# Kernel optimization log

Hardware: AMD Instinct MI355X
Metric: run time of the kernel (lower is better)

## Reference

```python
import jax, jax.numpy as jnp
import numpy as np

N_NODES = 100000
N_EDGES = 1250000
HID = 64
IN_CH = 64
OUT_CH = 16
N_GRAPHS = 512


def setup_inputs() -> dict:
    key = jax.random.key(0)
    ks = jax.random.split(key, 20)
    x = jax.random.normal(ks[0], (N_NODES, IN_CH), dtype=jnp.float32)
    edge_index = jax.random.randint(ks[1], (2, N_EDGES), 0, N_NODES, dtype=jnp.int64)
    batch = jnp.sort(jax.random.randint(ks[2], (N_NODES,), 0, N_GRAPHS, dtype=jnp.int64))
    s_in = 1.0 / np.sqrt(IN_CH)
    s_h = 1.0 / np.sqrt(HID)
    u = lambda k, shp, s: jax.random.uniform(k, shp, jnp.float32, -s, s)
    return {
        "x": x, "edge_index": edge_index, "batch": batch,
        "W0": u(ks[3], (IN_CH, HID), s_in), "b0": u(ks[4], (HID,), s_in),
        "W1a": u(ks[5], (HID, HID), s_h), "b1a": u(ks[6], (HID,), s_h),
        "W1b": u(ks[7], (HID, HID), s_h), "b1b": u(ks[8], (HID,), s_h),
        "W2a": u(ks[9], (HID, HID), s_h), "b2a": u(ks[10], (HID,), s_h),
        "W2b": u(ks[11], (HID, HID), s_h), "b2b": u(ks[12], (HID,), s_h),
        "W3a": u(ks[13], (HID, HID), s_h), "b3a": u(ks[14], (HID,), s_h),
        "W3b": u(ks[15], (HID, HID), s_h), "b3b": u(ks[16], (HID,), s_h),
        "Wl": u(ks[17], (HID, OUT_CH), s_h), "bl": u(ks[18], (OUT_CH,), s_h),
    }


def _gin_conv(h, src, dst, Wa, ba, Wb, bb):
    # GINConv, eps=0: mlp(x_i + sum_{j->i} x_j); mlp = Linear,ReLU,Linear
    agg = jax.ops.segment_sum(h[src], dst, num_segments=N_NODES)  # [N, HID]
    z = h + agg
    return jax.nn.relu(z @ Wa + ba) @ Wb + bb


def reference(x, edge_index, batch, W0, b0, W1a, b1a, W1b, b1b,
              W2a, b2a, W2b, b2b, W3a, b3a, W3b, b3b, Wl, bl):
    src, dst = edge_index[0], edge_index[1]
    h = jax.nn.relu(x @ W0 + b0)
    h = jax.nn.relu(_gin_conv(h, src, dst, W1a, b1a, W1b, b1b))
    h = jax.nn.relu(_gin_conv(h, src, dst, W2a, b2a, W2b, b2b))
    h = jax.nn.relu(_gin_conv(h, src, dst, W3a, b3a, W3b, b3b))
    # global mean pool over graphs
    sums = jax.ops.segment_sum(h, batch, num_segments=N_GRAPHS)  # [G, HID]
    cnts = jax.ops.segment_sum(jnp.ones((N_NODES,), h.dtype), batch, num_segments=N_GRAPHS)
    pooled = sums / jnp.maximum(cnts, 1.0)[:, None]
    # dropout p=0.5 is identity in eval mode
    return pooled @ Wl + bl  # [G, OUT_CH]
```

## Files before the change

### kernel.cpp

```cpp
#include <hip/hip_runtime.h>
#include <hip/hip_fp16.h>

#define N_NODES 100000
#define N_EDGES 1250000
#define HID 64
#define N_GRAPHS 512
#define OUT_CH 16

#define NSUP 196
#define SB_CAP 8192
#define E_BLK 2048
#define NPB ((N_EDGES + E_BLK - 1) / E_BLK)
#define TILE2 ((N_NODES + 127) / 128)
#define TSTRIDE 68

typedef _Float16 h16;
typedef _Float16 half2_t __attribute__((ext_vector_type(2)));
typedef _Float16 f16x8 __attribute__((ext_vector_type(8)));
typedef float f32x4 __attribute__((ext_vector_type(4)));

__device__ __forceinline__ void acc4(uint2 u, float& a0, float& a1, float& a2, float& a3) {
    half2_t h0 = __builtin_bit_cast(half2_t, u.x);
    half2_t h1 = __builtin_bit_cast(half2_t, u.y);
    a0 += (float)h0[0];
    a1 += (float)h0[1];
    a2 += (float)h1[0];
    a3 += (float)h1[1];
}

__device__ __forceinline__ unsigned pack2(float x, float y) {
    half2_t o;
    o[0] = (h16)x;
    o[1] = (h16)y;
    return __builtin_bit_cast(unsigned, o);
}

__global__ __launch_bounds__(256) void k_partition(const int* __restrict__ src,
                                                   const int* __restrict__ dst,
                                                   int* __restrict__ cnt,
                                                   int* __restrict__ buckets) {
    __shared__ int hist[256];
    __shared__ int gbase[256];
    __shared__ int tsum[256];
    __shared__ int stage[E_BLK];
    int t = threadIdx.x;
    int e0 = blockIdx.x * E_BLK;
    int eN = N_EDGES - e0;
    if (eN > E_BLK) eN = E_BLK;

    hist[t] = 0;
    __syncthreads();
    for (int i = t; i < eN; i += 256) atomicAdd(&hist[dst[e0 + i] >> 9], 1);
    __syncthreads();

    int c = hist[t];
    tsum[t] = c;
    __syncthreads();
    for (int off = 1; off < 256; off <<= 1) {
        int u = (t >= off) ? tsum[t - off] : 0;
        __syncthreads();
        tsum[t] += u;
        __syncthreads();
    }
    int pref = tsum[t] - c;
    if (t < NSUP && c > 0) gbase[t] = atomicAdd(&cnt[t], c);
    hist[t] = pref;
    __syncthreads();

    for (int i = t; i < eN; i += 256) {
        int s = src[e0 + i];
        int d = dst[e0 + i];
        int p = atomicAdd(&hist[d >> 9], 1);
        stage[p] = ((d & 511) << 17) | s;
    }
    __syncthreads();

    if (t < NSUP && c > 0) {
        int lstart = hist[t] - c;
        int gb = gbase[t];
        int cap = SB_CAP - gb;
        int n = c < cap ? c : (cap > 0 ? cap : 0);
        int* dp = buckets + (size_t)t * SB_CAP + gb;
        int r = 0;
        while (r < n && (((size_t)(dp + r)) & 15)) { dp[r] = stage[lstart + r]; ++r; }
        for (; r + 4 <= n; r += 4) {
            int4 v;
            v.x = stage[lstart + r];
            v.y = stage[lstart + r + 1];
            v.z = stage[lstart + r + 2];
            v.w = stage[lstart + r + 3];
            *(int4*)(dp + r) = v;
        }
        for (; r < n; ++r) dp[r] = stage[lstart + r];
    }
}

__global__ __launch_bounds__(256) void k_sort(const int* __restrict__ cnt,
                                              int* __restrict__ buckets,
                                              int* __restrict__ rowptrS) {
    __shared__ int srt[SB_CAP];
    __shared__ int hist[512];
    __shared__ int curs[512];
    __shared__ int tsum[256];
    int s = blockIdx.x, t = threadIdx.x;
    int n = cnt[s];
    n = n < SB_CAP ? n : SB_CAP;
    int* gb = buckets + (size_t)s * SB_CAP;
    int sBase = s * SB_CAP;

    hist[t] = 0;
    hist[t + 256] = 0;
    __syncthreads();
    for (int i = t; i < n; i += 256) atomicAdd(&hist[gb[i] >> 17], 1);
    __syncthreads();

    int c0 = hist[2 * t], c1 = hist[2 * t + 1];
    int tot = c0 + c1;
    tsum[t] = tot;
    __syncthreads();
    for (int off = 1; off < 256; off <<= 1) {
        int u = (t >= off) ? tsum[t - off] : 0;
        __syncthreads();
        tsum[t] += u;
        __syncthreads();
    }
    int pref = tsum[t] - tot;
    curs[2 * t] = pref;
    curs[2 * t + 1] = pref + c0;
    rowptrS[s * 513 + 2 * t] = sBase + pref;
    rowptrS[s * 513 + 2 * t + 1] = sBase + pref + c0;
    if (t == 255) rowptrS[s * 513 + 512] = sBase + n;
    __syncthreads();

    for (int i = t; i < n; i += 256) {
        int rec = gb[i];
        int pos = atomicAdd(&curs[rec >> 17], 1);
        srt[pos] = rec;
    }
    __syncthreads();
    for (int i = t; i < n; i += 256) gb[i] = srt[i];
}

__global__ __launch_bounds__(256) void k_aggregate(const int* __restrict__ rowptrS,
                                                   const int* __restrict__ buckets,
                                                   const h16* __restrict__ H,
                                                   h16* __restrict__ Z) {
    const uint2* H4 = (const uint2*)H;
    uint2* Z4 = (uint2*)Z;
    int lane = threadIdx.x & 63;
    int part = lane >> 4, sub = lane & 15;
    int gwave = (blockIdx.x * 256 + threadIdx.x) >> 6;
    int nw = (gridDim.x * 256) >> 6;
    for (int i0 = gwave * 4; i0 < N_NODES; i0 += nw * 4) {
        int i = i0 + part;
        bool valid = i < N_NODES;
        int iv = valid ? i : N_NODES - 1;
        int s = iv >> 9, l = iv & 511;
        int start = rowptrS[s * 513 + l];
        int end = valid ? rowptrS[s * 513 + l + 1] : start;
        float a0 = 0.f, a1 = 0.f, a2 = 0.f, a3 = 0.f;
        acc4(H4[(size_t)iv * 16 + sub], a0, a1, a2, a3);
        int j = start;
        for (; j + 8 <= end; j += 8) {
            int s0 = buckets[j] & 0x1FFFF;
            int s1 = buckets[j + 1] & 0x1FFFF;
            int s2 = buckets[j + 2] & 0x1FFFF;
            int s3 = buckets[j + 3] & 0x1FFFF;
            int s4 = buckets[j + 4] & 0x1FFFF;
            int s5 = buckets[j + 5] & 0x1FFFF;
            int s6 = buckets[j + 6] & 0x1FFFF;
            int s7 = buckets[j + 7] & 0x1FFFF;
            uint2 u0 = H4[(size_t)s0 * 16 + sub];
            uint2 u1 = H4[(size_t)s1 * 16 + sub];
            uint2 u2 = H4[(size_t)s2 * 16 + sub];
            uint2 u3 = H4[(size_t)s3 * 16 + sub];
            uint2 u4 = H4[(size_t)s4 * 16 + sub];
            uint2 u5 = H4[(size_t)s5 * 16 + sub];
            uint2 u6 = H4[(size_t)s6 * 16 + sub];
            uint2 u7 = H4[(size_t)s7 * 16 + sub];
            acc4(u0, a0, a1, a2, a3);
            acc4(u1, a0, a1, a2, a3);
            acc4(u2, a0, a1, a2, a3);
            acc4(u3, a0, a1, a2, a3);
            acc4(u4, a0, a1, a2, a3);
            acc4(u5, a0, a1, a2, a3);
            acc4(u6, a0, a1, a2, a3);
            acc4(u7, a0, a1, a2, a3);
        }
        if (j + 4 <= end) {
            int s0 = buckets[j] & 0x1FFFF;
            int s1 = buckets[j + 1] & 0x1FFFF;
            int s2 = buckets[j + 2] & 0x1FFFF;
            int s3 = buckets[j + 3] & 0x1FFFF;
            uint2 u0 = H4[(size_t)s0 * 16 + sub];
            uint2 u1 = H4[(size_t)s1 * 16 + sub];
            uint2 u2 = H4[(size_t)s2 * 16 + sub];
            uint2 u3 = H4[(size_t)s3 * 16 + sub];
            acc4(u0, a0, a1, a2, a3);
            acc4(u1, a0, a1, a2, a3);
            acc4(u2, a0, a1, a2, a3);
            acc4(u3, a0, a1, a2, a3);
            j += 4;
        }
        if (j + 2 <= end) {
            int s0 = buckets[j] & 0x1FFFF;
            int s1 = buckets[j + 1] & 0x1FFFF;
            uint2 u0 = H4[(size_t)s0 * 16 + sub];
            uint2 u1 = H4[(size_t)s1 * 16 + sub];
            acc4(u0, a0, a1, a2, a3);
            acc4(u1, a0, a1, a2, a3);
            j += 2;
        }
        if (j < end) {
            int s0 = buckets[j] & 0x1FFFF;
            acc4(H4[(size_t)s0 * 16 + sub], a0, a1, a2, a3);
        }
        if (valid) {
            uint2 o;
            o.x = pack2(a0, a1);
            o.y = pack2(a2, a3);
            Z4[(size_t)i * 16 + sub] = o;
        }
    }
}

__global__ __launch_bounds__(256) void k_wprep(const float* __restrict__ Wq0,
                                               const float* __restrict__ Wq1,
                                               const float* __restrict__ Wq2,
                                               const float* __restrict__ Wq3,
                                               const float* __restrict__ Wq4,
                                               const float* __restrict__ Wq5,
                                               const float* __restrict__ Wq6,
                                               h16* __restrict__ WF) {
    const float* Ws[7] = {Wq0, Wq1, Wq2, Wq3, Wq4, Wq5, Wq6};
    const float* W = Ws[blockIdx.x];
    h16* dstW = WF + (size_t)blockIdx.x * 4096;
    int t = threadIdx.x;
#pragma unroll
    for (int i = 0; i < 16; ++i) {
        int s = t + 256 * i;
        int k = s >> 6, col = s & 63;
        int kc = k >> 5, quad = (k >> 3) & 3, j = k & 7;
        int c = col >> 4, n = col & 15;
        dstW[((c * 2 + kc) * 4 + quad) * 128 + n * 8 + j] = (h16)W[s];
    }
}

__global__ __launch_bounds__(256) void k_mlp(const h16* __restrict__ WaF,
                                             const float* __restrict__ Ba,
                                             const h16* __restrict__ WbF,
                                             const float* __restrict__ Bb,
                                             const h16* __restrict__ Zin,
                                             h16* __restrict__ Hout) {
    __shared__ float sT[4 * 16 * TSTRIDE];
    int t = threadIdx.x;
    int w = t >> 6, lane = t & 63;
    int n16 = lane & 15, quad = lane >> 4;
    float* T = sT + w * 16 * TSTRIDE;

    f16x8 bwa[4][2], bwb[4][2];
#pragma unroll
    for (int c = 0; c < 4; ++c)
#pragma unroll
        for (int kc = 0; kc < 2; ++kc) {
            int f = ((c * 2 + kc) * 4 + quad) * 128 + n16 * 8;
            bwa[c][kc] = *(const f16x8*)(WaF + f);
            bwb[c][kc] = *(const f16x8*)(WbF + f);
        }
    float bva[4], bvb[4];
#pragma unroll
    for (int c = 0; c < 4; ++c) {
        bva[c] = Ba[c * 16 + n16];
        bvb[c] = Bb[c * 16 + n16];
    }

#pragma unroll
    for (int tt = 0; tt < 2; ++tt) {
        int rbase = blockIdx.x * 128 + tt * 64 + w * 16;
        int arow = rbase + n16;
        int crow = arow < N_NODES ? arow : N_NODES - 1;
        const f16x8* zp = (const f16x8*)(Zin + (size_t)crow * HID + quad * 8);
        f16x8 a0 = zp[0];
        f16x8 a1 = zp[4];

        f32x4 acc[4];
#pragma unroll
        for (int c = 0; c < 4; ++c) {
            acc[c] = (f32x4){bva[c], bva[c], bva[c], bva[c]};
            acc[c] = __builtin_amdgcn_mfma_f32_16x16x32_f16(a0, bwa[c][0], acc[c], 0, 0, 0);
            acc[c] = __builtin_amdgcn_mfma_f32_16x16x32_f16(a1, bwa[c][1], acc[c], 0, 0, 0);
        }

#pragma unroll
        for (int c = 0; c < 4; ++c)
#pragma unroll
            for (int r = 0; r < 4; ++r)
                T[(quad * 4 + r) * TSTRIDE + c * 16 + n16] = fmaxf(acc[c][r], 0.f);

        f16x8 ta[2];
#pragma unroll
        for (int kc = 0; kc < 2; ++kc) {
            float4 p = *(const float4*)&T[n16 * TSTRIDE + kc * 32 + quad * 8];
            float4 q = *(const float4*)&T[n16 * TSTRIDE + kc * 32 + quad * 8 + 4];
            f16x8 v;
            v[0] = (h16)p.x; v[1] = (h16)p.y; v[2] = (h16)p.z; v[3] = (h16)p.w;
            v[4] = (h16)q.x; v[5] = (h16)q.y; v[6] = (h16)q.z; v[7] = (h16)q.w;
            ta[kc] = v;
        }

#pragma unroll
        for (int c = 0; c < 4; ++c) {
            acc[c] = (f32x4){bvb[c], bvb[c], bvb[c], bvb[c]};
            acc[c] = __builtin_amdgcn_mfma_f32_16x16x32_f16(ta[0], bwb[c][0], acc[c], 0, 0, 0);
            acc[c] = __builtin_amdgcn_mfma_f32_16x16x32_f16(ta[1], bwb[c][1], acc[c], 0, 0, 0);
        }

#pragma unroll
        for (int c = 0; c < 4; ++c)
#pragma unroll
            for (int r = 0; r < 4; ++r)
                T[(quad * 4 + r) * TSTRIDE + c * 16 + n16] = fmaxf(acc[c][r], 0.f);
        {
            int rl = lane >> 2, seg = lane & 3;
            int row = rbase + rl;
            if (row < N_NODES) {
                const float* tr = &T[rl * TSTRIDE + seg * 16];
                f16x8 o0, o1;
#pragma unroll
                for (int i = 0; i < 8; ++i) {
                    o0[i] = (h16)tr[i];
                    o1[i] = (h16)tr[8 + i];
                }
                f16x8* dp = (f16x8*)(Hout + (size_t)row * HID + seg * 16);
                dp[0] = o0;
                dp[1] = o1;
            }
        }
    }
}

__global__ __launch_bounds__(256) void k_lin(const h16* __restrict__ W0F,
                                             const float* __restrict__ B,
                                             const float* __restrict__ Xin,
                                             h16* __restrict__ Hout) {
    __shared__ float sT[4 * 16 * TSTRIDE];
    int t = threadIdx.x;
    int w = t >> 6, lane = t & 63;
    int n16 = lane & 15, quad = lane >> 4;
    float* T = sT + w * 16 * TSTRIDE;

    f16x8 bw[4][2];
#pragma unroll
    for (int c = 0; c < 4; ++c)
#pragma unroll
        for (int kc = 0; kc < 2; ++kc)
            bw[c][kc] = *(const f16x8*)(W0F + ((c * 2 + kc) * 4 + quad) * 128 + n16 * 8);
    float bv[4];
#pragma unroll
    for (int c = 0; c < 4; ++c) bv[c] = B[c * 16 + n16];

#pragma unroll
    for (int tt = 0; tt < 2; ++tt) {
        int rbase = blockIdx.x * 128 + tt * 64 + w * 16;
        int arow = rbase + n16;
        int crow = arow < N_NODES ? arow : N_NODES - 1;
        f16x8 a[2];
#pragma unroll
        for (int kc = 0; kc < 2; ++kc) {
            const float4* xp = (const float4*)(Xin + (size_t)crow * HID + kc * 32 + quad * 8);
            float4 p = xp[0], q = xp[1];
            f16x8 v;
            v[0] = (h16)p.x; v[1] = (h16)p.y; v[2] = (h16)p.z; v[3] = (h16)p.w;
            v[4] = (h16)q.x; v[5] = (h16)q.y; v[6] = (h16)q.z; v[7] = (h16)q.w;
            a[kc] = v;
        }

        f32x4 acc[4];
#pragma unroll
        for (int c = 0; c < 4; ++c) {
            acc[c] = (f32x4){bv[c], bv[c], bv[c], bv[c]};
#pragma unroll
            for (int kc = 0; kc < 2; ++kc)
                acc[c] = __builtin_amdgcn_mfma_f32_16x16x32_f16(a[kc], bw[c][kc], acc[c], 0, 0, 0);
        }

#pragma unroll
        for (int c = 0; c < 4; ++c)
#pragma unroll
            for (int r = 0; r < 4; ++r)
                T[(quad * 4 + r) * TSTRIDE + c * 16 + n16] = fmaxf(acc[c][r], 0.f);
        {
            int rl = lane >> 2, seg = lane & 3;
            int row = rbase + rl;
            if (row < N_NODES) {
                const float* tr = &T[rl * TSTRIDE + seg * 16];
                f16x8 o0, o1;
#pragma unroll
                for (int i = 0; i < 8; ++i) {
                    o0[i] = (h16)tr[i];
                    o1[i] = (h16)tr[8 + i];
                }
                f16x8* dp = (f16x8*)(Hout + (size_t)row * HID + seg * 16);
                dp[0] = o0;
                dp[1] = o1;
            }
        }
    }
}

__global__ __launch_bounds__(256) void k_poolfinal(const h16* __restrict__ H,
                                                   const int* __restrict__ batch,
                                                   const float* __restrict__ Wl,
                                                   const float* __restrict__ bl,
                                                   float* __restrict__ out) {
    __shared__ float sp[4 * HID];
    int g = blockIdx.x;
    int t = threadIdx.x;
    int lane = t & 63, w = t >> 6;
    int lo = 0, hi = N_NODES;
    while (lo < hi) { int m = (lo + hi) >> 1; if (batch[m] < g) lo = m + 1; else hi = m; }
    int start = lo;
    hi = N_NODES;
    while (lo < hi) { int m = (lo + hi) >> 1; if (batch[m] < g + 1) lo = m + 1; else hi = m; }
    int end = lo;
    float s0 = 0.f, s1 = 0.f, s2 = 0.f, s3 = 0.f;
    int r = start + w;
    for (; r + 12 < end; r += 16) {
        float v0 = (float)H[(size_t)r * HID + lane];
        float v1 = (float)H[(size_t)(r + 4) * HID + lane];
        float v2 = (float)H[(size_t)(r + 8) * HID + lane];
        float v3 = (float)H[(size_t)(r + 12) * HID + lane];
        s0 += v0; s1 += v1; s2 += v2; s3 += v3;
    }
    for (; r < end; r += 4) s0 += (float)H[(size_t)r * HID + lane];
    sp[w * HID + lane] = s0 + s1 + s2 + s3;
    __syncthreads();
    if (t < HID) {
        float tot = sp[t] + sp[HID + t] + sp[2 * HID + t] + sp[3 * HID + t];
        float c = (end > start) ? (float)(end - start) : 1.0f;
        sp[t] = tot / c;
    }
    __syncthreads();
    if (t < OUT_CH) {
        float acc = bl[t];
#pragma unroll
        for (int k = 0; k < HID; ++k) acc += sp[k] * Wl[k * OUT_CH + t];
        out[g * OUT_CH + t] = acc;
    }
}

extern "C" void kernel_launch(void* const* d_in, const int* in_sizes, int n_in,
                              void* d_out, int out_size, void* d_ws, size_t ws_size,
                              hipStream_t stream) {
    const float* x     = (const float*)d_in[0];
    const int*   edge  = (const int*)d_in[1];
    const int*   batch = (const int*)d_in[2];
    const float* W0  = (const float*)d_in[3];
    const float* b0  = (const float*)d_in[4];
    const float* W1a = (const float*)d_in[5];
    const float* b1a = (const float*)d_in[6];
    const float* W1b = (const float*)d_in[7];
    const float* b1b = (const float*)d_in[8];
    const float* W2a = (const float*)d_in[9];
    const float* b2a = (const float*)d_in[10];
    const float* W2b = (const float*)d_in[11];
    const float* b2b = (const float*)d_in[12];
    const float* W3a = (const float*)d_in[13];
    const float* b3a = (const float*)d_in[14];
    const float* W3b = (const float*)d_in[15];
    const float* b3b = (const float*)d_in[16];
    const float* Wl  = (const float*)d_in[17];
    const float* bl  = (const float*)d_in[18];
    float* out = (float*)d_out;

    const int* src = edge;
    const int* dst = edge + N_EDGES;

    h16* HA = (h16*)d_ws;
    h16* Z  = HA + (size_t)N_NODES * HID;
    int* cnt     = (int*)(Z + (size_t)N_NODES * HID);
    int* rowptrS = cnt + NSUP;
    int* buckets = rowptrS + NSUP * 513;
    h16* WF      = (h16*)(buckets + (size_t)NSUP * SB_CAP);
    h16* W0F = WF;
    h16* W1aF = WF + 4096 * 1;
    h16* W1bF = WF + 4096 * 2;
    h16* W2aF = WF + 4096 * 3;
    h16* W2bF = WF + 4096 * 4;
    h16* W3aF = WF + 4096 * 5;
    h16* W3bF = WF + 4096 * 6;

    hipMemsetAsync(cnt, 0, NSUP * sizeof(int), stream);
    k_partition<<<NPB, 256, 0, stream>>>(src, dst, cnt, buckets);
    k_sort<<<NSUP, 256, 0, stream>>>(cnt, buckets, rowptrS);
    k_wprep<<<7, 256, 0, stream>>>(W0, W1a, W1b, W2a, W2b, W3a, W3b, WF);

    k_lin<<<TILE2, 256, 0, stream>>>(W0F, b0, x, HA);

    k_aggregate<<<6250, 256, 0, stream>>>(rowptrS, buckets, HA, Z);
    k_mlp<<<TILE2, 256, 0, stream>>>(W1aF, b1a, W1bF, b1b, Z, HA);

    k_aggregate<<<6250, 256, 0, stream>>>(rowptrS, buckets, HA, Z);
    k_mlp<<<TILE2, 256, 0, stream>>>(W2aF, b2a, W2bF, b2b, Z, HA);

    k_aggregate<<<6250, 256, 0, stream>>>(rowptrS, buckets, HA, Z);
    k_mlp<<<TILE2, 256, 0, stream>>>(W3aF, b3a, W3bF, b3b, Z, HA);

    k_poolfinal<<<N_GRAPHS, 256, 0, stream>>>(HA, batch, Wl, bl, out);
}
```

Baseline: 285.2 us.

## Fuse aggregation with GIN MLP and merge setup kernels into one launch

```diff
diff --git a/kernel.cpp b/kernel.cpp
--- a/kernel.cpp
+++ b/kernel.cpp
@@ -12,6 +12,7 @@
 #define E_BLK 2048
 #define NPB ((N_EDGES + E_BLK - 1) / E_BLK)
 #define TILE2 ((N_NODES + 127) / 128)
+#define NWP 6
 #define TSTRIDE 68
 
 typedef _Float16 h16;
@@ -35,63 +36,160 @@
     return __builtin_bit_cast(unsigned, o);
 }
 
-__global__ __launch_bounds__(256) void k_partition(const int* __restrict__ src,
-                                                   const int* __restrict__ dst,
-                                                   int* __restrict__ cnt,
-                                                   int* __restrict__ buckets) {
+__global__ __launch_bounds__(256) void k_fat(const int* __restrict__ src,
+                                             const int* __restrict__ dst,
+                                             int* __restrict__ cnt,
+                                             int* __restrict__ buckets,
+                                             const float* __restrict__ W1a,
+                                             const float* __restrict__ W1b,
+                                             const float* __restrict__ W2a,
+                                             const float* __restrict__ W2b,
+                                             const float* __restrict__ W3a,
+                                             const float* __restrict__ W3b,
+                                             h16* __restrict__ WF,
+                                             const float* __restrict__ W0,
+                                             const float* __restrict__ B0,
+                                             const float* __restrict__ Xin,
+                                             h16* __restrict__ Hout) {
     __shared__ int hist[256];
     __shared__ int gbase[256];
     __shared__ int tsum[256];
-    __shared__ int stage[E_BLK];
+    __shared__ __align__(16) int stage[E_BLK];
+    __shared__ __align__(16) float sT[4 * 16 * TSTRIDE];
+
+    int b = blockIdx.x;
     int t = threadIdx.x;
-    int e0 = blockIdx.x * E_BLK;
-    int eN = N_EDGES - e0;
-    if (eN > E_BLK) eN = E_BLK;
-
-    hist[t] = 0;
-    __syncthreads();
-    for (int i = t; i < eN; i += 256) atomicAdd(&hist[dst[e0 + i] >> 9], 1);
-    __syncthreads();
-
-    int c = hist[t];
-    tsum[t] = c;
-    __syncthreads();
-    for (int off = 1; off < 256; off <<= 1) {
-        int u = (t >= off) ? tsum[t - off] : 0;
-        __syncthreads();
-        tsum[t] += u;
-        __syncthreads();
-    }
-    int pref = tsum[t] - c;
-    if (t < NSUP && c > 0) gbase[t] = atomicAdd(&cnt[t], c);
-    hist[t] = pref;
-    __syncthreads();
-
-    for (int i = t; i < eN; i += 256) {
-        int s = src[e0 + i];
-        int d = dst[e0 + i];
-        int p = atomicAdd(&hist[d >> 9], 1);
-        stage[p] = ((d & 511) << 17) | s;
-    }
-    __syncthreads();
-
-    if (t < NSUP && c > 0) {
-        int lstart = hist[t] - c;
-        int gb = gbase[t];
-        int cap = SB_CAP - gb;
-        int n = c < cap ? c : (cap > 0 ? cap : 0);
-        int* dp = buckets + (size_t)t * SB_CAP + gb;
-        int r = 0;
-        while (r < n && (((size_t)(dp + r)) & 15)) { dp[r] = stage[lstart + r]; ++r; }
-        for (; r + 4 <= n; r += 4) {
-            int4 v;
-            v.x = stage[lstart + r];
-            v.y = stage[lstart + r + 1];
-            v.z = stage[lstart + r + 2];
-            v.w = stage[lstart + r + 3];
-            *(int4*)(dp + r) = v;
-        }
-        for (; r < n; ++r) dp[r] = stage[lstart + r];
+
+    if (b < NPB) {
+        int e0 = b * E_BLK;
+        int eN = N_EDGES - e0;
+        if (eN > E_BLK) eN = E_BLK;
+
+        hist[t] = 0;
+        __syncthreads();
+        for (int i = t; i < eN; i += 256) atomicAdd(&hist[dst[e0 + i] >> 9], 1);
+        __syncthreads();
+
+        int c = hist[t];
+        tsum[t] = c;
+        __syncthreads();
+        for (int off = 1; off < 256; off <<= 1) {
+            int u = (t >= off) ? tsum[t - off] : 0;
+            __syncthreads();
+            tsum[t] += u;
+            __syncthreads();
+        }
+        int pref = tsum[t] - c;
+        if (t < NSUP && c > 0) gbase[t] = atomicAdd(&cnt[t], c);
+        hist[t] = pref;
+        __syncthreads();
+
+        for (int i = t; i < eN; i += 256) {
+            int s = src[e0 + i];
+            int d = dst[e0 + i];
+            int p = atomicAdd(&hist[d >> 9], 1);
+            stage[p] = ((d & 511) << 17) | s;
+        }
+        __syncthreads();
+
+        if (t < NSUP && c > 0) {
+            int lstart = hist[t] - c;
+            int gb = gbase[t];
+            int cap = SB_CAP - gb;
+            int n = c < cap ? c : (cap > 0 ? cap : 0);
+            int* dp = buckets + (size_t)t * SB_CAP + gb;
+            int r = 0;
+            while (r < n && (((size_t)(dp + r)) & 15)) { dp[r] = stage[lstart + r]; ++r; }
+            for (; r + 4 <= n; r += 4) {
+                int4 v;
+                v.x = stage[lstart + r];
+                v.y = stage[lstart + r + 1];
+                v.z = stage[lstart + r + 2];
+                v.w = stage[lstart + r + 3];
+                *(int4*)(dp + r) = v;
+            }
+            for (; r < n; ++r) dp[r] = stage[lstart + r];
+        }
+    } else if (b < NPB + NWP) {
+        const float* Ws[NWP] = {W1a, W1b, W2a, W2b, W3a, W3b};
+        const float* W = Ws[b - NPB];
+        h16* dstW = WF + (size_t)(b - NPB) * 4096;
+#pragma unroll
+        for (int i = 0; i < 16; ++i) {
+            int s = t + 256 * i;
+            int k = s >> 6, col = s & 63;
+            int kc = k >> 5, quad = (k >> 3) & 3, j = k & 7;
+            int c = col >> 4, n = col & 15;
+            dstW[((c * 2 + kc) * 4 + quad) * 128 + n * 8 + j] = (h16)W[s];
+        }
+    } else {
+        int lb = b - NPB - NWP;
+        int w = t >> 6, lane = t & 63;
+        int n16 = lane & 15, quad = lane >> 4;
+        float* T = sT + w * 16 * TSTRIDE;
+
+        f16x8 bw[4][2];
+#pragma unroll
+        for (int c = 0; c < 4; ++c)
+#pragma unroll
+            for (int kc = 0; kc < 2; ++kc) {
+                f16x8 v;
+#pragma unroll
+                for (int j = 0; j < 8; ++j)
+                    v[j] = (h16)W0[(kc * 32 + quad * 8 + j) * 64 + c * 16 + n16];
+                bw[c][kc] = v;
+            }
+        float bv[4];
+#pragma unroll
+        for (int c = 0; c < 4; ++c) bv[c] = B0[c * 16 + n16];
+
+#pragma unroll
+        for (int tt = 0; tt < 2; ++tt) {
+            int rbase = lb * 128 + tt * 64 + w * 16;
+            int arow = rbase + n16;
+            int crow = arow < N_NODES ? arow : N_NODES - 1;
+            f16x8 a[2];
+#pragma unroll
+            for (int kc = 0; kc < 2; ++kc) {
+                const float4* xp = (const float4*)(Xin + (size_t)crow * HID + kc * 32 + quad * 8);
+                float4 p = xp[0], q = xp[1];
+                f16x8 v;
+                v[0] = (h16)p.x; v[1] = (h16)p.y; v[2] = (h16)p.z; v[3] = (h16)p.w;
+                v[4] = (h16)q.x; v[5] = (h16)q.y; v[6] = (h16)q.z; v[7] = (h16)q.w;
+                a[kc] = v;
+            }
+
+            f32x4 acc[4];
+#pragma unroll
+            for (int c = 0; c < 4; ++c) {
+                acc[c] = (f32x4){bv[c], bv[c], bv[c], bv[c]};
+#pragma unroll
+                for (int kc = 0; kc < 2; ++kc)
+                    acc[c] = __builtin_amdgcn_mfma_f32_16x16x32_f16(a[kc], bw[c][kc], acc[c], 0, 0, 0);
+            }
+
+#pragma unroll
+            for (int c = 0; c < 4; ++c)
+#pragma unroll
+                for (int r = 0; r < 4; ++r)
+                    T[(quad * 4 + r) * TSTRIDE + c * 16 + n16] = fmaxf(acc[c][r], 0.f);
+            {
+                int rl = lane >> 2, seg = lane & 3;
+                int row = rbase + rl;
+                if (row < N_NODES) {
+                    const float* tr = &T[rl * TSTRIDE + seg * 16];
+                    f16x8 o0, o1;
+#pragma unroll
+                    for (int i = 0; i < 8; ++i) {
+                        o0[i] = (h16)tr[i];
+                        o1[i] = (h16)tr[8 + i];
+                    }
+                    f16x8* dp = (f16x8*)(Hout + (size_t)row * HID + seg * 16);
+                    dp[0] = o0;
+                    dp[1] = o1;
+                }
+            }
+        }
     }
 }
 
@@ -141,20 +239,27 @@
     for (int i = t; i < n; i += 256) gb[i] = srt[i];
 }
 
-__global__ __launch_bounds__(256) void k_aggregate(const int* __restrict__ rowptrS,
-                                                   const int* __restrict__ buckets,
-                                                   const h16* __restrict__ H,
-                                                   h16* __restrict__ Z) {
-    const uint2* H4 = (const uint2*)H;
-    uint2* Z4 = (uint2*)Z;
-    int lane = threadIdx.x & 63;
+__global__ __launch_bounds__(256) void k_aggmlp(const int* __restrict__ rowptrS,
+                                                const int* __restrict__ buckets,
+                                                const h16* __restrict__ WaF,
+                                                const float* __restrict__ Ba,
+                                                const h16* __restrict__ WbF,
+                                                const float* __restrict__ Bb,
+                                                const h16* __restrict__ Hin,
+                                                h16* __restrict__ Hout) {
+    __shared__ __align__(16) float sT[4 * 16 * TSTRIDE];
+    char* zb = (char*)sT;
+    const uint2* H4 = (const uint2*)Hin;
+    int t = threadIdx.x;
+    int w = t >> 6, lane = t & 63;
     int part = lane >> 4, sub = lane & 15;
-    int gwave = (blockIdx.x * 256 + threadIdx.x) >> 6;
-    int nw = (gridDim.x * 256) >> 6;
-    for (int i0 = gwave * 4; i0 < N_NODES; i0 += nw * 4) {
-        int i = i0 + part;
-        bool valid = i < N_NODES;
-        int iv = valid ? i : N_NODES - 1;
+    int n16 = lane & 15, quad = lane >> 4;
+
+    for (int it = 0; it < 8; ++it) {
+        int rloc = it * 16 + w * 4 + part;
+        int grow = blockIdx.x * 128 + rloc;
+        bool valid = grow < N_NODES;
+        int iv = valid ? grow : N_NODES - 1;
         int s = iv >> 9, l = iv & 511;
         int start = rowptrS[s * 513 + l];
         int end = valid ? rowptrS[s * 513 + l + 1] : start;
@@ -215,48 +320,22 @@
             int s0 = buckets[j] & 0x1FFFF;
             acc4(H4[(size_t)s0 * 16 + sub], a0, a1, a2, a3);
         }
-        if (valid) {
-            uint2 o;
-            o.x = pack2(a0, a1);
-            o.y = pack2(a2, a3);
-            Z4[(size_t)i * 16 + sub] = o;
-        }
-    }
-}
-
-__global__ __launch_bounds__(256) void k_wprep(const float* __restrict__ Wq0,
-                                               const float* __restrict__ Wq1,
-                                               const float* __restrict__ Wq2,
-                                               const float* __restrict__ Wq3,
-                                               const float* __restrict__ Wq4,
-                                               const float* __restrict__ Wq5,
-                                               const float* __restrict__ Wq6,
-                                               h16* __restrict__ WF) {
-    const float* Ws[7] = {Wq0, Wq1, Wq2, Wq3, Wq4, Wq5, Wq6};
-    const float* W = Ws[blockIdx.x];
-    h16* dstW = WF + (size_t)blockIdx.x * 4096;
-    int t = threadIdx.x;
-#pragma unroll
-    for (int i = 0; i < 16; ++i) {
-        int s = t + 256 * i;
-        int k = s >> 6, col = s & 63;
-        int kc = k >> 5, quad = (k >> 3) & 3, j = k & 7;
-        int c = col >> 4, n = col & 15;
-        dstW[((c * 2 + kc) * 4 + quad) * 128 + n * 8 + j] = (h16)W[s];
-    }
-}
-
-__global__ __launch_bounds__(256) void k_mlp(const h16* __restrict__ WaF,
-                                             const float* __restrict__ Ba,
-                                             const h16* __restrict__ WbF,
-                                             const float* __restrict__ Bb,
-                                             const h16* __restrict__ Zin,
-                                             h16* __restrict__ Hout) {
-    __shared__ float sT[4 * 16 * TSTRIDE];
-    int t = threadIdx.x;
-    int w = t >> 6, lane = t & 63;
-    int n16 = lane & 15, quad = lane >> 4;
-    float* T = sT + w * 16 * TSTRIDE;
+        uint2 o;
+        o.x = pack2(a0, a1);
+        o.y = pack2(a2, a3);
+        int zoff = (rloc * 128 + sub * 8) ^ ((rloc & 7) << 4);
+        *(uint2*)(zb + zoff) = o;
+    }
+    __syncthreads();
+
+    f16x8 afr[2][2];
+#pragma unroll
+    for (int tt = 0; tt < 2; ++tt) {
+        int rl = tt * 64 + w * 16 + n16;
+        int swz = (rl & 7) << 4;
+        afr[tt][0] = *(const f16x8*)(zb + ((rl * 128 + quad * 16) ^ swz));
+        afr[tt][1] = *(const f16x8*)(zb + ((rl * 128 + 64 + quad * 16) ^ swz));
+    }
 
     f16x8 bwa[4][2], bwb[4][2];
 #pragma unroll
@@ -273,22 +352,19 @@
         bva[c] = Ba[c * 16 + n16];
         bvb[c] = Bb[c * 16 + n16];
     }
-
+    __syncthreads();
+
+    float* T = sT + w * 16 * TSTRIDE;
 #pragma unroll
     for (int tt = 0; tt < 2; ++tt) {
         int rbase = blockIdx.x * 128 + tt * 64 + w * 16;
-        int arow = rbase + n16;
-        int crow = arow < N_NODES ? arow : N_NODES - 1;
-        const f16x8* zp = (const f16x8*)(Zin + (size_t)crow * HID + quad * 8);
-        f16x8 a0 = zp[0];
-        f16x8 a1 = zp[4];
 
         f32x4 acc[4];
 #pragma unroll
         for (int c = 0; c < 4; ++c) {
             acc[c] = (f32x4){bva[c], bva[c], bva[c], bva[c]};
-            acc[c] = __builtin_amdgcn_mfma_f32_16x16x32_f16(a0, bwa[c][0], acc[c], 0, 0, 0);
-            acc[c] = __builtin_amdgcn_mfma_f32_16x16x32_f16(a1, bwa[c][1], acc[c], 0, 0, 0);
+            acc[c] = __builtin_amdgcn_mfma_f32_16x16x32_f16(afr[tt][0], bwa[c][0], acc[c], 0, 0, 0);
+            acc[c] = __builtin_amdgcn_mfma_f32_16x16x32_f16(afr[tt][1], bwa[c][1], acc[c], 0, 0, 0);
         }
 
 #pragma unroll
@@ -313,75 +389,6 @@
             acc[c] = (f32x4){bvb[c], bvb[c], bvb[c], bvb[c]};
             acc[c] = __builtin_amdgcn_mfma_f32_16x16x32_f16(ta[0], bwb[c][0], acc[c], 0, 0, 0);
             acc[c] = __builtin_amdgcn_mfma_f32_16x16x32_f16(ta[1], bwb[c][1], acc[c], 0, 0, 0);
-        }
-
-#pragma unroll
-        for (int c = 0; c < 4; ++c)
-#pragma unroll
-            for (int r = 0; r < 4; ++r)
-                T[(quad * 4 + r) * TSTRIDE + c * 16 + n16] = fmaxf(acc[c][r], 0.f);
-        {
-            int rl = lane >> 2, seg = lane & 3;
-            int row = rbase + rl;
-            if (row < N_NODES) {
-                const float* tr = &T[rl * TSTRIDE + seg * 16];
-                f16x8 o0, o1;
-#pragma unroll
-                for (int i = 0; i < 8; ++i) {
-                    o0[i] = (h16)tr[i];
-                    o1[i] = (h16)tr[8 + i];
-                }
-                f16x8* dp = (f16x8*)(Hout + (size_t)row * HID + seg * 16);
-                dp[0] = o0;
-                dp[1] = o1;
-            }
-        }
-    }
-}
-
-__global__ __launch_bounds__(256) void k_lin(const h16* __restrict__ W0F,
-                                             const float* __restrict__ B,
-                                             const float* __restrict__ Xin,
-                                             h16* __restrict__ Hout) {
-    __shared__ float sT[4 * 16 * TSTRIDE];
-    int t = threadIdx.x;
-    int w = t >> 6, lane = t & 63;
-    int n16 = lane & 15, quad = lane >> 4;
-    float* T = sT + w * 16 * TSTRIDE;
-
-    f16x8 bw[4][2];
-#pragma unroll
-    for (int c = 0; c < 4; ++c)
-#pragma unroll
-        for (int kc = 0; kc < 2; ++kc)
-            bw[c][kc] = *(const f16x8*)(W0F + ((c * 2 + kc) * 4 + quad) * 128 + n16 * 8);
-    float bv[4];
-#pragma unroll
-    for (int c = 0; c < 4; ++c) bv[c] = B[c * 16 + n16];
-
-#pragma unroll
-    for (int tt = 0; tt < 2; ++tt) {
-        int rbase = blockIdx.x * 128 + tt * 64 + w * 16;
-        int arow = rbase + n16;
-        int crow = arow < N_NODES ? arow : N_NODES - 1;
-        f16x8 a[2];
-#pragma unroll
-        for (int kc = 0; kc < 2; ++kc) {
-            const float4* xp = (const float4*)(Xin + (size_t)crow * HID + kc * 32 + quad * 8);
-            float4 p = xp[0], q = xp[1];
-            f16x8 v;
-            v[0] = (h16)p.x; v[1] = (h16)p.y; v[2] = (h16)p.z; v[3] = (h16)p.w;
-            v[4] = (h16)q.x; v[5] = (h16)q.y; v[6] = (h16)q.z; v[7] = (h16)q.w;
-            a[kc] = v;
-        }
-
-        f32x4 acc[4];
-#pragma unroll
-        for (int c = 0; c < 4; ++c) {
-            acc[c] = (f32x4){bv[c], bv[c], bv[c], bv[c]};
-#pragma unroll
-            for (int kc = 0; kc < 2; ++kc)
-                acc[c] = __builtin_amdgcn_mfma_f32_16x16x32_f16(a[kc], bw[c][kc], acc[c], 0, 0, 0);
         }
 
 #pragma unroll
@@ -477,34 +484,26 @@
     const int* dst = edge + N_EDGES;
 
     h16* HA = (h16*)d_ws;
-    h16* Z  = HA + (size_t)N_NODES * HID;
-    int* cnt     = (int*)(Z + (size_t)N_NODES * HID);
+    h16* HB = HA + (size_t)N_NODES * HID;
+    int* cnt     = (int*)(HB + (size_t)N_NODES * HID);
     int* rowptrS = cnt + NSUP;
     int* buckets = rowptrS + NSUP * 513;
     h16* WF      = (h16*)(buckets + (size_t)NSUP * SB_CAP);
-    h16* W0F = WF;
-    h16* W1aF = WF + 4096 * 1;
-    h16* W1bF = WF + 4096 * 2;
-    h16* W2aF = WF + 4096 * 3;
-    h16* W2bF = WF + 4096 * 4;
-    h16* W3aF = WF + 4096 * 5;
-    h16* W3bF = WF + 4096 * 6;
+    h16* W1aF = WF;
+    h16* W1bF = WF + 4096 * 1;
+    h16* W2aF = WF + 4096 * 2;
+    h16* W2bF = WF + 4096 * 3;
+    h16* W3aF = WF + 4096 * 4;
+    h16* W3bF = WF + 4096 * 5;
 
     hipMemsetAsync(cnt, 0, NSUP * sizeof(int), stream);
-    k_partition<<<NPB, 256, 0, stream>>>(src, dst, cnt, buckets);
+    k_fat<<<NPB + NWP + TILE2, 256, 0, stream>>>(src, dst, cnt, buckets,
+        W1a, W1b, W2a, W2b, W3a, W3b, WF, W0, b0, x, HA);
     k_sort<<<NSUP, 256, 0, stream>>>(cnt, buckets, rowptrS);
-    k_wprep<<<7, 256, 0, stream>>>(W0, W1a, W1b, W2a, W2b, W3a, W3b, WF);
-
-    k_lin<<<TILE2, 256, 0, stream>>>(W0F, b0, x, HA);
-
-    k_aggregate<<<6250, 256, 0, stream>>>(rowptrS, buckets, HA, Z);
-    k_mlp<<<TILE2, 256, 0, stream>>>(W1aF, b1a, W1bF, b1b, Z, HA);
-
-    k_aggregate<<<6250, 256, 0, stream>>>(rowptrS, buckets, HA, Z);
-    k_mlp<<<TILE2, 256, 0, stream>>>(W2aF, b2a, W2bF, b2b, Z, HA);
-
-    k_aggregate<<<6250, 256, 0, stream>>>(rowptrS, buckets, HA, Z);
-    k_mlp<<<TILE2, 256, 0, stream>>>(W3aF, b3a, W3bF, b3b, Z, HA);
-
-    k_poolfinal<<<N_GRAPHS, 256, 0, stream>>>(HA, batch, Wl, bl, out);
-}
+
+    k_aggmlp<<<TILE2, 256, 0, stream>>>(rowptrS, buckets, W1aF, b1a, W1bF, b1b, HA, HB);
+    k_aggmlp<<<TILE2, 256, 0, stream>>>(rowptrS, buckets, W2aF, b2a, W2bF, b2b, HB, HA);
+    k_aggmlp<<<TILE2, 256, 0, stream>>>(rowptrS, buckets, W3aF, b3a, W3bF, b3b, HA, HB);
+
+    k_poolfinal<<<N_GRAPHS, 256, 0, stream>>>(HB, batch, Wl, bl, out);
+}
```

Result: slower. 365.0 us (+28.0%).
